# Kernel tuning notes

Hardware: AMD Instinct MI355X
Metric: run time of the kernel (lower is better)

Reference implementation:

```python
import jax, jax.numpy as jnp
import numpy as np

C_EM, H_EM, C_A = 256, 8, 32
S, R = 1024, 256
LN_EPS = 1e-5
MASK_BIAS = 1e9


def setup_inputs() -> dict:
    key = jax.random.key(0)
    ks = jax.random.split(key, 8)
    sc = 0.02
    m = jax.random.normal(ks[0], (S, R, C_EM), jnp.float32)
    # binary column mask (float mask in the original; int here so it is a constant)
    mask = (jax.random.uniform(ks[1], (S, R)) < 0.9).astype(jnp.int32)
    return {
        "m": m,
        "ln_g": jnp.ones((C_EM,), jnp.float32),
        "ln_b": jnp.zeros((C_EM,), jnp.float32),
        "w_q": jax.random.normal(ks[2], (C_EM, H_EM, C_A), jnp.float32) * sc,
        "w_k": jax.random.normal(ks[3], (C_EM, C_A), jnp.float32) * sc,
        "w_v": jax.random.normal(ks[4], (C_EM, C_A), jnp.float32) * sc,
        "w_g": jax.random.normal(ks[5], (C_EM, H_EM, C_A), jnp.float32) * sc,
        "b_g": jnp.zeros((H_EM, C_A), jnp.float32),
        "w_o": jax.random.normal(ks[6], (H_EM, C_A, C_EM), jnp.float32) * sc,
        "b_o": jnp.zeros((C_EM,), jnp.float32),
        "mask": mask,
    }


def reference(m, ln_g, ln_b, w_q, w_k, w_v, w_g, b_g, w_o, b_o, mask):
    maskf = mask.astype(m.dtype)  # [s, r]
    # LayerNorm over c_em (biased variance, eps=1e-5, torch default)
    mu = jnp.mean(m, axis=-1, keepdims=True)
    var = jnp.mean((m - mu) ** 2, axis=-1, keepdims=True)
    x = (m - mu) * jax.lax.rsqrt(var + LN_EPS) * ln_g + ln_b  # [s, r, c]
    # masked mean-pool over s -> per-column query
    q_pool = jnp.sum(x * maskf[..., None], axis=-3) / (jnp.sum(maskf, axis=-2)[..., None] + 1e-10)  # [r, c]
    Q = jnp.einsum('rc,chd->rhd', q_pool, w_q) * (1.0 / np.sqrt(C_A))  # [r, h, d]
    K = jnp.einsum('src,cd->srd', x, w_k)  # [s, r, d]
    V = jnp.einsum('src,cd->srd', x, w_v)  # [s, r, d]
    G = jax.nn.sigmoid(jnp.einsum('src,chd->srhd', x, w_g) + b_g)  # [s, r, h, d]
    bias = (maskf - 1.0) * MASK_BIAS  # [s, r]
    logits = jnp.einsum('rhd,srd->srh', Q, K) + bias[..., None]  # [s, r, h]
    A = jax.nn.softmax(logits, axis=-3)  # softmax over s
    O = jnp.einsum('srh,srd->rhd', A, V)  # [r, h, d]
    out = jnp.einsum('srhd,hdc->src', O[None, :, :, :] * G, w_o) + b_o  # [s, r, c]
    return out
```

## Files before the change

### kernel.cpp

```cpp
#include <hip/hip_runtime.h>
#include <math.h>

#define S_DIM 1024
#define R_DIM 256
#define C_DIM 256
#define SCALE 0.17677669529663687f

typedef short bf16x8 __attribute__((ext_vector_type(8)));
typedef float f32x4 __attribute__((ext_vector_type(4)));

__device__ __forceinline__ float wred(float v) {
#pragma unroll
  for (int m = 32; m >= 1; m >>= 1) v += __shfl_xor(v, m, 64);
  return v;
}

__device__ __forceinline__ short f2bf(float f) {
  union { float f; unsigned u; } v;
  v.f = f;
  unsigned r = v.u + 0x7fffu + ((v.u >> 16) & 1u);
  return (short)(r >> 16);
}

__device__ __forceinline__ float bf2f(short s) {
  union { unsigned u; float f; } v;
  v.u = ((unsigned)(unsigned short)s) << 16;
  return v.f;
}

__device__ __forceinline__ float fast_sigmoid_mul(float o, float gl) {
  return o * __builtin_amdgcn_rcpf(1.f + __expf(-gl));
}

__global__ __launch_bounds__(256)
void k0_prep(const float* __restrict__ w_g, const float* __restrict__ w_o,
             const float* __restrict__ w_k, const float* __restrict__ w_v,
             short* __restrict__ wgB, short* __restrict__ woB,
             short* __restrict__ wkvB) {
  const int id = blockIdx.x * 256 + threadIdx.x;
  if (id < 16384) {
    const int which = id >> 13;
    const int s = id & 8191;
    const int n = s & 255, g = (s >> 8) & 3, kb = s >> 10;
    const float* W = which ? w_o : w_g;
    short* Out = which ? woB : wgB;
#pragma unroll
    for (int j = 0; j < 8; ++j)
      Out[(((size_t)kb * 256 + n) * 4 + g) * 8 + j] =
          f2bf(W[(size_t)(kb * 32 + g * 8 + j) * 256 + n]);
  } else {
    const int s = id - 16384;
    const int n = s & 63, g = (s >> 6) & 3, kb = s >> 8;
    const float* W = (n < 32) ? w_k : w_v;
    const int nn = n & 31;
#pragma unroll
    for (int j = 0; j < 8; ++j)
      wkvB[(((size_t)kb * 64 + n) * 4 + g) * 8 + j] =
          f2bf(W[(size_t)(kb * 32 + g * 8 + j) * 32 + nn]);
  }
}

__global__ __launch_bounds__(256, 3)
void k1_ln_kv(const float* __restrict__ mIn, const float* __restrict__ ln_g,
              const float* __restrict__ ln_b, const short* __restrict__ wkvB,
              const int* __restrict__ mask,
              float* __restrict__ K_ws, float* __restrict__ V_ws,
              float* __restrict__ pool_ws, char* __restrict__ xout) {
  __shared__ __align__(16) short A_lds[2048 * 8];
  __shared__ float mask_s[64];
  __shared__ float4 poolp[4][64];
  const int r  = blockIdx.y;
  const int s0 = blockIdx.x * 64;
  const int t  = threadIdx.x;

  if (t < 64) mask_s[t] = mask[(s0 + t) * R_DIM + r] ? 1.f : 0.f;

  {
    const int rw = t >> 2;
    const int q  = t & 3;
    const size_t p = (size_t)(s0 + rw) * R_DIM + r;
    const float* src = mIn + p * C_DIM + q * 64;
    float4 xv[16];
    float sum = 0.f, ssq = 0.f;
#pragma unroll
    for (int i = 0; i < 16; ++i) {
      xv[i] = *(const float4*)(src + i * 4);
      sum += xv[i].x + xv[i].y + xv[i].z + xv[i].w;
      ssq += xv[i].x * xv[i].x + xv[i].y * xv[i].y + xv[i].z * xv[i].z +
             xv[i].w * xv[i].w;
    }
    sum += __shfl_xor(sum, 1, 64); ssq += __shfl_xor(ssq, 1, 64);
    sum += __shfl_xor(sum, 2, 64); ssq += __shfl_xor(ssq, 2, 64);
    const float mu = sum * (1.f / 256.f);
    const float var = ssq * (1.f / 256.f) - mu * mu;
    const float rs = rsqrtf(var + 1e-5f);

    const int gw = rw >> 4;
    const int lf0 = rw & 15;
#pragma unroll
    for (int kh = 0; kh < 2; ++kh) {
      const int kb = 2 * q + kh;
#pragma unroll
      for (int g = 0; g < 4; ++g) {
        const int lidx = kh * 32 + g * 8;
        const float4 a0 = xv[lidx >> 2], a1 = xv[(lidx >> 2) + 1];
        const float4 g0 = *(const float4*)(ln_g + kb * 32 + g * 8);
        const float4 g1 = *(const float4*)(ln_g + kb * 32 + g * 8 + 4);
        const float4 b0 = *(const float4*)(ln_b + kb * 32 + g * 8);
        const float4 b1 = *(const float4*)(ln_b + kb * 32 + g * 8 + 4);
        bf16x8 f;
        f[0] = f2bf((a0.x - mu) * rs * g0.x + b0.x);
        f[1] = f2bf((a0.y - mu) * rs * g0.y + b0.y);
        f[2] = f2bf((a0.z - mu) * rs * g0.z + b0.z);
        f[3] = f2bf((a0.w - mu) * rs * g0.w + b0.w);
        f[4] = f2bf((a1.x - mu) * rs * g1.x + b1.x);
        f[5] = f2bf((a1.y - mu) * rs * g1.y + b1.y);
        f[6] = f2bf((a1.z - mu) * rs * g1.z + b1.z);
        f[7] = f2bf((a1.w - mu) * rs * g1.w + b1.w);
        int byte = (((gw * 8 + kb) * 64 + lf0 + g * 16) << 4) ^ (((kb >> 1) & 3) << 5);
        *(bf16x8*)((char*)A_lds + byte) = f;
      }
    }
  }
  __syncthreads();

  {
    const int w = t >> 6, l = t & 63;
    const int lm = l & 15, g = l >> 4;
    f32x4 acc[4];
#pragma unroll
    for (int ni = 0; ni < 4; ++ni) acc[ni] = (f32x4){0.f, 0.f, 0.f, 0.f};
#pragma unroll
    for (int kb = 0; kb < 8; ++kb) {
      const int byte = (((w * 8 + kb) * 64 + l) << 4) ^ (((kb >> 1) & 3) << 5);
      const bf16x8 a = *(const bf16x8*)((char*)A_lds + byte);
      bf16x8 bfr[4];
#pragma unroll
      for (int ni = 0; ni < 4; ++ni)
        bfr[ni] = *(const bf16x8*)(wkvB + (((size_t)kb * 64 + lm + ni * 16) * 4 + g) * 8);
#pragma unroll
      for (int ni = 0; ni < 4; ++ni)
        acc[ni] = __builtin_amdgcn_mfma_f32_16x16x32_bf16(a, bfr[ni], acc[ni], 0, 0, 0);
    }
#pragma unroll
    for (int ni = 0; ni < 4; ++ni) {
      const int col = lm + ni * 16;
      float* Out = (col < 32) ? K_ws : V_ws;
      const int cc = col & 31;
#pragma unroll
      for (int reg = 0; reg < 4; ++reg) {
        const int s = s0 + w * 16 + g * 4 + reg;
        Out[((size_t)s * R_DIM + r) * 32 + cc] = acc[ni][reg];
      }
    }
  }

#pragma unroll
  for (int i = 0; i < 8; ++i) {
    const int u = i * 256 + t;
    const bf16x8 v = *(const bf16x8*)((const char*)A_lds + u * 16);
    *(bf16x8*)(xout + ((size_t)((s0 + (u >> 5)) * R_DIM + r)) * 1024 +
               (u & 31) * 16) = v;
  }

  {
    const int lc = t & 63;
    const int wq = t >> 6;
    const int kb = lc >> 3, g2 = (lc >> 1) & 3, bh = (lc & 1) * 4;
    float4 ps = make_float4(0.f, 0.f, 0.f, 0.f);
    for (int i = 0; i < 16; ++i) {
      const int rloc = (i + lc) & 15;
      const int byte =
          ((((wq * 8 + kb) * 64 + rloc + g2 * 16) << 4) + bh * 2) ^ (((kb >> 1) & 3) << 5);
      const short4 xb = *(const short4*)((char*)A_lds + byte);
      const float mk = mask_s[wq * 16 + rloc];
      ps.x += mk * bf2f(xb.x);
      ps.y += mk * bf2f(xb.y);
      ps.z += mk * bf2f(xb.z);
      ps.w += mk * bf2f(xb.w);
    }
    poolp[wq][lc] = ps;
  }
  __syncthreads();
  if (t < 64) {
    const float4 a = poolp[0][t], b = poolp[1][t], c = poolp[2][t], d = poolp[3][t];
    atomicAdd(&pool_ws[r * C_DIM + t * 4 + 0], a.x + b.x + c.x + d.x);
    atomicAdd(&pool_ws[r * C_DIM + t * 4 + 1], a.y + b.y + c.y + d.y);
    atomicAdd(&pool_ws[r * C_DIM + t * 4 + 2], a.z + b.z + c.z + d.z);
    atomicAdd(&pool_ws[r * C_DIM + t * 4 + 3], a.w + b.w + c.w + d.w);
  }
}

__global__ __launch_bounds__(256, 2)
void k2_q(const float* __restrict__ pool_ws, const int* __restrict__ mask,
          const float* __restrict__ w_q, float* __restrict__ Q_ws) {
  __shared__ float qp[256];
  __shared__ float wsum[4];
  const int r = blockIdx.x, t = threadIdx.x;
  int cnt = 0;
  for (int s = t; s < S_DIM; s += 256) cnt += mask[s * R_DIM + r];
  float cf = wred((float)cnt);
  if ((t & 63) == 0) wsum[t >> 6] = cf;
  __syncthreads();
  const float denom = wsum[0] + wsum[1] + wsum[2] + wsum[3] + 1e-10f;
  qp[t] = pool_ws[r * C_DIM + t] / denom;
  __syncthreads();
  float acc = 0.f;
  for (int c = 0; c < 256; ++c) acc += qp[c] * w_q[c * 256 + t];
  Q_ws[r * 256 + t] = acc * SCALE;
}

__global__ __launch_bounds__(256, 2)
void k3_attn(const float* __restrict__ K_ws, const float* __restrict__ V_ws,
             const int* __restrict__ mask, const float* __restrict__ Q_ws,
             float* __restrict__ O_ws) {
  __shared__ float q[256];
  __shared__ float lg[1024 * 9];
  __shared__ float kv[256 * 36];
  __shared__ float mh[8], inv[8];
  const int r = blockIdx.x, t = threadIdx.x;
  q[t] = Q_ws[r * 256 + t];

  for (int ch = 0; ch < 4; ++ch) {
    const int sb = ch * 256;
    __syncthreads();
    for (int f = t; f < 2048; f += 256) {
      const int sl = f >> 3, dq = f & 7;
      *(float4*)(kv + sl * 36 + dq * 4) =
          *(const float4*)(K_ws + ((size_t)(sb + sl) * R_DIM + r) * 32 + dq * 4);
    }
    __syncthreads();
    float kr[32];
#pragma unroll
    for (int dq = 0; dq < 8; ++dq)
      *(float4*)(kr + dq * 4) = *(float4*)(kv + t * 36 + dq * 4);
    const float bias = mask[(sb + t) * R_DIM + r] ? 0.f : -1e9f;
#pragma unroll
    for (int h = 0; h < 8; ++h) {
      float a = 0.f;
#pragma unroll
      for (int d = 0; d < 32; ++d) a += q[h * 32 + d] * kr[d];
      lg[(sb + t) * 9 + h] = a + bias;
    }
  }
  __syncthreads();
  {
    const int h = t >> 5, l32 = t & 31;
    float mx = -INFINITY;
    for (int k = 0; k < 32; ++k) mx = fmaxf(mx, lg[(l32 + 32 * k) * 9 + h]);
#pragma unroll
    for (int mk = 16; mk >= 1; mk >>= 1) mx = fmaxf(mx, __shfl_xor(mx, mk, 64));
    float sm = 0.f;
    for (int k = 0; k < 32; ++k) sm += __expf(lg[(l32 + 32 * k) * 9 + h] - mx);
#pragma unroll
    for (int mk = 16; mk >= 1; mk >>= 1) sm += __shfl_xor(sm, mk, 64);
    if (l32 == 0) { mh[h] = mx; inv[h] = 1.f / sm; }
  }
  __syncthreads();
  for (int f = t; f < 8192; f += 256) {
    const int s = f >> 3, h = f & 7;
    lg[s * 9 + h] = __expf(lg[s * 9 + h] - mh[h]) * inv[h];
  }
  const int h = t >> 5, d = t & 31;
  float o = 0.f;
  for (int ch = 0; ch < 4; ++ch) {
    const int sb = ch * 256;
    __syncthreads();
    for (int f = t; f < 2048; f += 256) {
      const int sl = f >> 3, dq = f & 7;
      *(float4*)(kv + sl * 36 + dq * 4) =
          *(const float4*)(V_ws + ((size_t)(sb + sl) * R_DIM + r) * 32 + dq * 4);
    }
    __syncthreads();
    for (int sl = 0; sl < 256; ++sl)
      o += lg[(sb + sl) * 9 + h] * kv[sl * 36 + d];
  }
  O_ws[r * 256 + t] = o;
}

__global__ __launch_bounds__(256, 4)
void k4_mfma(const short* __restrict__ wgB, const float* __restrict__ b_g,
             const float* __restrict__ O_ws, const short* __restrict__ woB,
             const float* __restrict__ b_o, float* __restrict__ outx) {
  __shared__ __align__(16) short A_lds[2048 * 8];
  const int t = threadIdx.x;
  const int s0 = blockIdx.x * 64;
  const int r  = blockIdx.y;
  const int l = t & 63, w = t >> 6, lm = l & 15, g = l >> 4;
  const char* glB = (const char*)outx;

  bf16x8 stg[8];
#pragma unroll
  for (int i = 0; i < 8; ++i) {
    const int u = i * 256 + t;
    stg[i] = *(const bf16x8*)(glB +
        ((size_t)((s0 + (u >> 5)) * R_DIM + r)) * 1024 + (u & 31) * 16);
  }
#pragma unroll
  for (int i = 0; i < 8; ++i)
    *(bf16x8*)((char*)A_lds + (i * 256 + t) * 16) = stg[i];
  __syncthreads();

  const int col = w * 64 + lm;
  float o4[4], bg4[4], bo4[4];
#pragma unroll
  for (int ni = 0; ni < 4; ++ni) {
    o4[ni]  = O_ws[r * 256 + col + ni * 16];
    bg4[ni] = b_g[col + ni * 16];
    bo4[ni] = b_o[col + ni * 16];
  }

  f32x4 acc[4][4];
#pragma unroll
  for (int ni = 0; ni < 4; ++ni)
#pragma unroll
    for (int mi = 0; mi < 4; ++mi)
      acc[mi][ni] = (f32x4){bg4[ni], bg4[ni], bg4[ni], bg4[ni]};

#pragma unroll
  for (int kb = 0; kb < 8; ++kb) {
    const int swz = ((kb >> 1) & 3) << 5;
    bf16x8 a[4], bb[4];
#pragma unroll
    for (int mi = 0; mi < 4; ++mi)
      a[mi] = *(const bf16x8*)((char*)A_lds + ((((mi * 8 + kb) * 64 + l) << 4) ^ swz));
#pragma unroll
    for (int ni = 0; ni < 4; ++ni)
      bb[ni] = *(const bf16x8*)(wgB + (((size_t)kb * 256 + col + ni * 16) * 4 + g) * 8);
#pragma unroll
    for (int mi = 0; mi < 4; ++mi)
#pragma unroll
      for (int ni = 0; ni < 4; ++ni)
        acc[mi][ni] = __builtin_amdgcn_mfma_f32_16x16x32_bf16(a[mi], bb[ni], acc[mi][ni], 0, 0, 0);
  }
  __syncthreads();

#pragma unroll
  for (int mi = 0; mi < 4; ++mi) {
#pragma unroll
    for (int ni = 0; ni < 4; ++ni) {
      const int c2 = col + ni * 16;
      const int kb2 = c2 >> 5, g2 = (c2 >> 3) & 3, b2 = c2 & 7;
#pragma unroll
      for (int reg = 0; reg < 4; ++reg) {
        const float tv = fast_sigmoid_mul(o4[ni], acc[mi][ni][reg]);
        const int u = (mi * 8 + kb2) * 64 + (g * 4 + reg) + g2 * 16;
        const int byte = ((u << 4) ^ (((u >> 4) & 3) << 4)) + b2 * 2;
        *(short*)((char*)A_lds + byte) = f2bf(tv);
      }
    }
  }
  __syncthreads();

#pragma unroll
  for (int ni = 0; ni < 4; ++ni)
#pragma unroll
    for (int mi = 0; mi < 4; ++mi)
      acc[mi][ni] = (f32x4){bo4[ni], bo4[ni], bo4[ni], bo4[ni]};
#pragma unroll
  for (int kb = 0; kb < 8; ++kb) {
    bf16x8 a[4], bb[4];
#pragma unroll
    for (int mi = 0; mi < 4; ++mi) {
      const int u = (mi * 8 + kb) * 64 + l;
      a[mi] = *(const bf16x8*)((char*)A_lds + ((u << 4) ^ (g << 4)));
    }
#pragma unroll
    for (int ni = 0; ni < 4; ++ni)
      bb[ni] = *(const bf16x8*)(woB + (((size_t)kb * 256 + col + ni * 16) * 4 + g) * 8);
#pragma unroll
    for (int mi = 0; mi < 4; ++mi)
#pragma unroll
      for (int ni = 0; ni < 4; ++ni)
        acc[mi][ni] = __builtin_amdgcn_mfma_f32_16x16x32_bf16(a[mi], bb[ni], acc[mi][ni], 0, 0, 0);
  }

#pragma unroll
  for (int mi = 0; mi < 4; ++mi)
#pragma unroll
    for (int ni = 0; ni < 4; ++ni)
#pragma unroll
      for (int reg = 0; reg < 4; ++reg) {
        const int row = mi * 16 + g * 4 + reg;
        outx[((size_t)((s0 + row) * R_DIM + r)) * 256 + col + ni * 16] =
            acc[mi][ni][reg];
      }
}

extern "C" void kernel_launch(void* const* d_in, const int* in_sizes, int n_in,
                              void* d_out, int out_size, void* d_ws, size_t ws_size,
                              hipStream_t stream) {
  const float* mIn  = (const float*)d_in[0];
  const float* ln_g = (const float*)d_in[1];
  const float* ln_b = (const float*)d_in[2];
  const float* w_q  = (const float*)d_in[3];
  const float* w_k  = (const float*)d_in[4];
  const float* w_v  = (const float*)d_in[5];
  const float* w_g  = (const float*)d_in[6];
  const float* b_g  = (const float*)d_in[7];
  const float* w_o  = (const float*)d_in[8];
  const float* b_o  = (const float*)d_in[9];
  const int*   mask = (const int*)d_in[10];
  float* outp = (float*)d_out;

  char* ws = (char*)d_ws;
  const size_t NP = (size_t)S_DIM * R_DIM;
  float* K_ws    = (float*)ws;
  float* V_ws    = K_ws + NP * 32;
  float* pool_ws = V_ws + NP * 32;
  float* Q_ws    = pool_ws + 65536;
  float* O_ws    = Q_ws + 65536;
  short* wgB     = (short*)(O_ws + 65536);
  short* woB     = wgB + 65536;
  short* wkvB    = woB + 65536;

  hipMemsetAsync(pool_ws, 0, 65536 * sizeof(float), stream);

  k0_prep<<<72, 256, 0, stream>>>(w_g, w_o, w_k, w_v, wgB, woB, wkvB);
  k1_ln_kv<<<dim3(S_DIM / 64, R_DIM), 256, 0, stream>>>(
      mIn, ln_g, ln_b, wkvB, mask, K_ws, V_ws, pool_ws, (char*)outp);
  k2_q<<<R_DIM, 256, 0, stream>>>(pool_ws, mask, w_q, Q_ws);
  k3_attn<<<R_DIM, 256, 0, stream>>>(K_ws, V_ws, mask, Q_ws, O_ws);
  k4_mfma<<<dim3(S_DIM / 64, R_DIM), 256, 0, stream>>>(
      wgB, b_g, O_ws, woB, b_o, outp);
}
```

Measured before the change: 393.6 us.

## Recompute LayerNorm in output kernel instead of staging bf16 activations

The first kernel no longer writes the normalized bf16 activations into the output buffer. It stores only per-row mean and inverse std. The gating/output kernel re-reads the fp32 input and recomputes the normalization on the fly, trading an intermediate write-plus-read for a second read of the larger fp32 input. Both kernels also halve the row tile from 64 to 32 and raise the occupancy hint. In k1 the waves are now split so half do the K/V MFMA work while the other half compute the masked pool.

Result: slower. 464.9 us (+18.1%).

```diff
diff --git a/kernel.cpp b/kernel.cpp
--- a/kernel.cpp
+++ b/kernel.cpp
@@ -60,30 +60,31 @@
   }
 }
 
-__global__ __launch_bounds__(256, 3)
+__global__ __launch_bounds__(256, 6)
 void k1_ln_kv(const float* __restrict__ mIn, const float* __restrict__ ln_g,
               const float* __restrict__ ln_b, const short* __restrict__ wkvB,
               const int* __restrict__ mask,
+              float* __restrict__ mu_ws, float* __restrict__ rs_ws,
               float* __restrict__ K_ws, float* __restrict__ V_ws,
-              float* __restrict__ pool_ws, char* __restrict__ xout) {
-  __shared__ __align__(16) short A_lds[2048 * 8];
-  __shared__ float mask_s[64];
-  __shared__ float4 poolp[4][64];
+              float* __restrict__ pool_ws) {
+  __shared__ __align__(16) short A_lds[1024 * 8];
+  __shared__ float mask_s[32];
+  __shared__ float4 poolp[2][64];
   const int r  = blockIdx.y;
-  const int s0 = blockIdx.x * 64;
+  const int s0 = blockIdx.x * 32;
   const int t  = threadIdx.x;
 
-  if (t < 64) mask_s[t] = mask[(s0 + t) * R_DIM + r] ? 1.f : 0.f;
+  if (t < 32) mask_s[t] = mask[(s0 + t) * R_DIM + r] ? 1.f : 0.f;
 
   {
-    const int rw = t >> 2;
-    const int q  = t & 3;
+    const int rw = t >> 3;
+    const int q  = t & 7;
     const size_t p = (size_t)(s0 + rw) * R_DIM + r;
-    const float* src = mIn + p * C_DIM + q * 64;
-    float4 xv[16];
+    const float* src = mIn + p * C_DIM + q * 32;
+    float4 xv[8];
     float sum = 0.f, ssq = 0.f;
 #pragma unroll
-    for (int i = 0; i < 16; ++i) {
+    for (int i = 0; i < 8; ++i) {
       xv[i] = *(const float4*)(src + i * 4);
       sum += xv[i].x + xv[i].y + xv[i].z + xv[i].w;
       ssq += xv[i].x * xv[i].x + xv[i].y * xv[i].y + xv[i].z * xv[i].z +
@@ -91,41 +92,40 @@
     }
     sum += __shfl_xor(sum, 1, 64); ssq += __shfl_xor(ssq, 1, 64);
     sum += __shfl_xor(sum, 2, 64); ssq += __shfl_xor(ssq, 2, 64);
+    sum += __shfl_xor(sum, 4, 64); ssq += __shfl_xor(ssq, 4, 64);
     const float mu = sum * (1.f / 256.f);
     const float var = ssq * (1.f / 256.f) - mu * mu;
     const float rs = rsqrtf(var + 1e-5f);
+    if (q == 0) { mu_ws[p] = mu; rs_ws[p] = rs; }
 
     const int gw = rw >> 4;
     const int lf0 = rw & 15;
-#pragma unroll
-    for (int kh = 0; kh < 2; ++kh) {
-      const int kb = 2 * q + kh;
-#pragma unroll
-      for (int g = 0; g < 4; ++g) {
-        const int lidx = kh * 32 + g * 8;
-        const float4 a0 = xv[lidx >> 2], a1 = xv[(lidx >> 2) + 1];
-        const float4 g0 = *(const float4*)(ln_g + kb * 32 + g * 8);
-        const float4 g1 = *(const float4*)(ln_g + kb * 32 + g * 8 + 4);
-        const float4 b0 = *(const float4*)(ln_b + kb * 32 + g * 8);
-        const float4 b1 = *(const float4*)(ln_b + kb * 32 + g * 8 + 4);
-        bf16x8 f;
-        f[0] = f2bf((a0.x - mu) * rs * g0.x + b0.x);
-        f[1] = f2bf((a0.y - mu) * rs * g0.y + b0.y);
-        f[2] = f2bf((a0.z - mu) * rs * g0.z + b0.z);
-        f[3] = f2bf((a0.w - mu) * rs * g0.w + b0.w);
-        f[4] = f2bf((a1.x - mu) * rs * g1.x + b1.x);
-        f[5] = f2bf((a1.y - mu) * rs * g1.y + b1.y);
-        f[6] = f2bf((a1.z - mu) * rs * g1.z + b1.z);
-        f[7] = f2bf((a1.w - mu) * rs * g1.w + b1.w);
-        int byte = (((gw * 8 + kb) * 64 + lf0 + g * 16) << 4) ^ (((kb >> 1) & 3) << 5);
-        *(bf16x8*)((char*)A_lds + byte) = f;
-      }
-    }
-  }
-  __syncthreads();
-
-  {
-    const int w = t >> 6, l = t & 63;
+    const int kb = q;
+    const int swz = ((kb >> 1) & 3) << 5;
+#pragma unroll
+    for (int g = 0; g < 4; ++g) {
+      const float4 a0 = xv[g * 2], a1 = xv[g * 2 + 1];
+      const float4 g0 = *(const float4*)(ln_g + kb * 32 + g * 8);
+      const float4 g1 = *(const float4*)(ln_g + kb * 32 + g * 8 + 4);
+      const float4 b0 = *(const float4*)(ln_b + kb * 32 + g * 8);
+      const float4 b1 = *(const float4*)(ln_b + kb * 32 + g * 8 + 4);
+      bf16x8 f;
+      f[0] = f2bf((a0.x - mu) * rs * g0.x + b0.x);
+      f[1] = f2bf((a0.y - mu) * rs * g0.y + b0.y);
+      f[2] = f2bf((a0.z - mu) * rs * g0.z + b0.z);
+      f[3] = f2bf((a0.w - mu) * rs * g0.w + b0.w);
+      f[4] = f2bf((a1.x - mu) * rs * g1.x + b1.x);
+      f[5] = f2bf((a1.y - mu) * rs * g1.y + b1.y);
+      f[6] = f2bf((a1.z - mu) * rs * g1.z + b1.z);
+      f[7] = f2bf((a1.w - mu) * rs * g1.w + b1.w);
+      const int byte = (((gw * 8 + kb) * 64 + lf0 + g * 16) << 4) ^ swz;
+      *(bf16x8*)((char*)A_lds + byte) = f;
+    }
+  }
+  __syncthreads();
+
+  const int w = t >> 6, l = t & 63;
+  if (w < 2) {
     const int lm = l & 15, g = l >> 4;
     f32x4 acc[4];
 #pragma unroll
@@ -153,19 +153,9 @@
         Out[((size_t)s * R_DIM + r) * 32 + cc] = acc[ni][reg];
       }
     }
-  }
-
-#pragma unroll
-  for (int i = 0; i < 8; ++i) {
-    const int u = i * 256 + t;
-    const bf16x8 v = *(const bf16x8*)((const char*)A_lds + u * 16);
-    *(bf16x8*)(xout + ((size_t)((s0 + (u >> 5)) * R_DIM + r)) * 1024 +
-               (u & 31) * 16) = v;
-  }
-
-  {
-    const int lc = t & 63;
-    const int wq = t >> 6;
+  } else {
+    const int wq = w - 2;
+    const int lc = l;
     const int kb = lc >> 3, g2 = (lc >> 1) & 3, bh = (lc & 1) * 4;
     float4 ps = make_float4(0.f, 0.f, 0.f, 0.f);
     for (int i = 0; i < 16; ++i) {
@@ -183,11 +173,11 @@
   }
   __syncthreads();
   if (t < 64) {
-    const float4 a = poolp[0][t], b = poolp[1][t], c = poolp[2][t], d = poolp[3][t];
-    atomicAdd(&pool_ws[r * C_DIM + t * 4 + 0], a.x + b.x + c.x + d.x);
-    atomicAdd(&pool_ws[r * C_DIM + t * 4 + 1], a.y + b.y + c.y + d.y);
-    atomicAdd(&pool_ws[r * C_DIM + t * 4 + 2], a.z + b.z + c.z + d.z);
-    atomicAdd(&pool_ws[r * C_DIM + t * 4 + 3], a.w + b.w + c.w + d.w);
+    const float4 a = poolp[0][t], b = poolp[1][t];
+    atomicAdd(&pool_ws[r * C_DIM + t * 4 + 0], a.x + b.x);
+    atomicAdd(&pool_ws[r * C_DIM + t * 4 + 1], a.y + b.y);
+    atomicAdd(&pool_ws[r * C_DIM + t * 4 + 2], a.z + b.z);
+    atomicAdd(&pool_ws[r * C_DIM + t * 4 + 3], a.w + b.w);
   }
 }
 
@@ -278,27 +268,48 @@
   O_ws[r * 256 + t] = o;
 }
 
-__global__ __launch_bounds__(256, 4)
-void k4_mfma(const short* __restrict__ wgB, const float* __restrict__ b_g,
-             const float* __restrict__ O_ws, const short* __restrict__ woB,
-             const float* __restrict__ b_o, float* __restrict__ outx) {
-  __shared__ __align__(16) short A_lds[2048 * 8];
+__global__ __launch_bounds__(256, 6)
+void k4_mfma(const float* __restrict__ mIn, const float* __restrict__ ln_g,
+             const float* __restrict__ ln_b, const float* __restrict__ mu_ws,
+             const float* __restrict__ rs_ws, const short* __restrict__ wgB,
+             const float* __restrict__ b_g, const float* __restrict__ O_ws,
+             const short* __restrict__ woB, const float* __restrict__ b_o,
+             float* __restrict__ out) {
+  __shared__ __align__(16) short A_lds[1024 * 8];
   const int t = threadIdx.x;
-  const int s0 = blockIdx.x * 64;
+  const int s0 = blockIdx.x * 32;
   const int r  = blockIdx.y;
   const int l = t & 63, w = t >> 6, lm = l & 15, g = l >> 4;
-  const char* glB = (const char*)outx;
-
-  bf16x8 stg[8];
-#pragma unroll
-  for (int i = 0; i < 8; ++i) {
-    const int u = i * 256 + t;
-    stg[i] = *(const bf16x8*)(glB +
-        ((size_t)((s0 + (u >> 5)) * R_DIM + r)) * 1024 + (u & 31) * 16);
-  }
-#pragma unroll
-  for (int i = 0; i < 8; ++i)
-    *(bf16x8*)((char*)A_lds + (i * 256 + t) * 16) = stg[i];
+
+  {
+    const int rw = t >> 3;
+    const int q  = t & 7;
+    const size_t p = (size_t)(s0 + rw) * R_DIM + r;
+    const float mu = mu_ws[p], rs = rs_ws[p];
+    const float* src = mIn + p * C_DIM + q * 32;
+    const int gw = rw >> 4, lf0 = rw & 15;
+    const int swz = ((q >> 1) & 3) << 5;
+#pragma unroll
+    for (int g4 = 0; g4 < 4; ++g4) {
+      const float4 m0 = *(const float4*)(src + g4 * 8);
+      const float4 m1 = *(const float4*)(src + g4 * 8 + 4);
+      const float4 g0 = *(const float4*)(ln_g + q * 32 + g4 * 8);
+      const float4 g1 = *(const float4*)(ln_g + q * 32 + g4 * 8 + 4);
+      const float4 b0 = *(const float4*)(ln_b + q * 32 + g4 * 8);
+      const float4 b1 = *(const float4*)(ln_b + q * 32 + g4 * 8 + 4);
+      bf16x8 f;
+      f[0] = f2bf((m0.x - mu) * rs * g0.x + b0.x);
+      f[1] = f2bf((m0.y - mu) * rs * g0.y + b0.y);
+      f[2] = f2bf((m0.z - mu) * rs * g0.z + b0.z);
+      f[3] = f2bf((m0.w - mu) * rs * g0.w + b0.w);
+      f[4] = f2bf((m1.x - mu) * rs * g1.x + b1.x);
+      f[5] = f2bf((m1.y - mu) * rs * g1.y + b1.y);
+      f[6] = f2bf((m1.z - mu) * rs * g1.z + b1.z);
+      f[7] = f2bf((m1.w - mu) * rs * g1.w + b1.w);
+      const int byte = (((gw * 8 + q) * 64 + lf0 + g4 * 16) << 4) ^ swz;
+      *(bf16x8*)((char*)A_lds + byte) = f;
+    }
+  }
   __syncthreads();
 
   const int col = w * 64 + lm;
@@ -310,25 +321,25 @@
     bo4[ni] = b_o[col + ni * 16];
   }
 
-  f32x4 acc[4][4];
+  f32x4 acc[2][4];
 #pragma unroll
   for (int ni = 0; ni < 4; ++ni)
 #pragma unroll
-    for (int mi = 0; mi < 4; ++mi)
+    for (int mi = 0; mi < 2; ++mi)
       acc[mi][ni] = (f32x4){bg4[ni], bg4[ni], bg4[ni], bg4[ni]};
 
 #pragma unroll
   for (int kb = 0; kb < 8; ++kb) {
     const int swz = ((kb >> 1) & 3) << 5;
-    bf16x8 a[4], bb[4];
-#pragma unroll
-    for (int mi = 0; mi < 4; ++mi)
+    bf16x8 a[2], bb[4];
+#pragma unroll
+    for (int mi = 0; mi < 2; ++mi)
       a[mi] = *(const bf16x8*)((char*)A_lds + ((((mi * 8 + kb) * 64 + l) << 4) ^ swz));
 #pragma unroll
     for (int ni = 0; ni < 4; ++ni)
       bb[ni] = *(const bf16x8*)(wgB + (((size_t)kb * 256 + col + ni * 16) * 4 + g) * 8);
 #pragma unroll
-    for (int mi = 0; mi < 4; ++mi)
+    for (int mi = 0; mi < 2; ++mi)
 #pragma unroll
       for (int ni = 0; ni < 4; ++ni)
         acc[mi][ni] = __builtin_amdgcn_mfma_f32_16x16x32_bf16(a[mi], bb[ni], acc[mi][ni], 0, 0, 0);
@@ -336,7 +347,7 @@
   __syncthreads();
 
 #pragma unroll
-  for (int mi = 0; mi < 4; ++mi) {
+  for (int mi = 0; mi < 2; ++mi) {
 #pragma unroll
     for (int ni = 0; ni < 4; ++ni) {
       const int c2 = col + ni * 16;
@@ -355,13 +366,13 @@
 #pragma unroll
   for (int ni = 0; ni < 4; ++ni)
 #pragma unroll
-    for (int mi = 0; mi < 4; ++mi)
+    for (int mi = 0; mi < 2; ++mi)
       acc[mi][ni] = (f32x4){bo4[ni], bo4[ni], bo4[ni], bo4[ni]};
 #pragma unroll
   for (int kb = 0; kb < 8; ++kb) {
-    bf16x8 a[4], bb[4];
-#pragma unroll
-    for (int mi = 0; mi < 4; ++mi) {
+    bf16x8 a[2], bb[4];
+#pragma unroll
+    for (int mi = 0; mi < 2; ++mi) {
       const int u = (mi * 8 + kb) * 64 + l;
       a[mi] = *(const bf16x8*)((char*)A_lds + ((u << 4) ^ (g << 4)));
     }
@@ -369,20 +380,20 @@
     for (int ni = 0; ni < 4; ++ni)
       bb[ni] = *(const bf16x8*)(woB + (((size_t)kb * 256 + col + ni * 16) * 4 + g) * 8);
 #pragma unroll
-    for (int mi = 0; mi < 4; ++mi)
+    for (int mi = 0; mi < 2; ++mi)
 #pragma unroll
       for (int ni = 0; ni < 4; ++ni)
         acc[mi][ni] = __builtin_amdgcn_mfma_f32_16x16x32_bf16(a[mi], bb[ni], acc[mi][ni], 0, 0, 0);
   }
 
 #pragma unroll
-  for (int mi = 0; mi < 4; ++mi)
+  for (int mi = 0; mi < 2; ++mi)
 #pragma unroll
     for (int ni = 0; ni < 4; ++ni)
 #pragma unroll
       for (int reg = 0; reg < 4; ++reg) {
         const int row = mi * 16 + g * 4 + reg;
-        outx[((size_t)((s0 + row) * R_DIM + r)) * 256 + col + ni * 16] =
+        out[((size_t)((s0 + row) * R_DIM + r)) * 256 + col + ni * 16] =
             acc[mi][ni][reg];
       }
 }
@@ -405,7 +416,9 @@
 
   char* ws = (char*)d_ws;
   const size_t NP = (size_t)S_DIM * R_DIM;
-  float* K_ws    = (float*)ws;
+  float* mu_ws   = (float*)ws;
+  float* rs_ws   = mu_ws + NP;
+  float* K_ws    = rs_ws + NP;
   float* V_ws    = K_ws + NP * 32;
   float* pool_ws = V_ws + NP * 32;
   float* Q_ws    = pool_ws + 65536;
@@ -417,10 +430,10 @@
   hipMemsetAsync(pool_ws, 0, 65536 * sizeof(float), stream);
 
   k0_prep<<<72, 256, 0, stream>>>(w_g, w_o, w_k, w_v, wgB, woB, wkvB);
-  k1_ln_kv<<<dim3(S_DIM / 64, R_DIM), 256, 0, stream>>>(
-      mIn, ln_g, ln_b, wkvB, mask, K_ws, V_ws, pool_ws, (char*)outp);
+  k1_ln_kv<<<dim3(S_DIM / 32, R_DIM), 256, 0, stream>>>(
+      mIn, ln_g, ln_b, wkvB, mask, mu_ws, rs_ws, K_ws, V_ws, pool_ws);
   k2_q<<<R_DIM, 256, 0, stream>>>(pool_ws, mask, w_q, Q_ws);
   k3_attn<<<R_DIM, 256, 0, stream>>>(K_ws, V_ws, mask, Q_ws, O_ws);
-  k4_mfma<<<dim3(S_DIM / 64, R_DIM), 256, 0, stream>>>(
-      wgB, b_g, O_ws, woB, b_o, outp);
-}
+  k4_mfma<<<dim3(S_DIM / 32, R_DIM), 256, 0, stream>>>(
+      mIn, ln_g, ln_b, mu_ws, rs_ws, wgB, b_g, O_ws, woB, b_o, outp);
+}
```
